# Kernel tuning notes

Hardware: AMD Instinct MI355X
Metric: run time of the kernel (lower is better)

## Reference

```python
import jax, jax.numpy as jnp
import numpy as np

N = 100000   # nodes
E = 1600000  # edges
DIN = 32     # node_in_channels
DE = 16      # edge_feature_dim
H = 64       # gnn_hidden_channels
L = 4        # num_gnn_layers
MH = 128     # mlp_hidden_channels
OUT = 10     # out_channels_final
G = 128      # graphs in batch
BN_EPS = 1e-5
GIN_EPS = 0.0


def setup_inputs() -> dict:
    key = jax.random.key(0)
    ks = jax.random.split(key, 24)
    s = 0.05
    return dict(
        x=jax.random.normal(ks[0], (N, DIN), jnp.float32),
        edge_index=jax.random.randint(ks[1], (2, E), 0, N),
        edge_attr=jax.random.normal(ks[2], (E, DE), jnp.float32),
        batch=jnp.sort(jax.random.randint(ks[3], (N,), 0, G)),
        # layer 0 (in = DIN)
        l0_edge_w=jax.random.normal(ks[4], (DIN, DE), jnp.float32) * s,
        l0_edge_b=jnp.zeros((DIN,), jnp.float32),
        l0_w1=jax.random.normal(ks[5], (H, DIN), jnp.float32) * s,
        l0_b1=jnp.zeros((H,), jnp.float32),
        l0_w2=jax.random.normal(ks[6], (H, H), jnp.float32) * s,
        l0_b2=jnp.zeros((H,), jnp.float32),
        # layers 1..L-1 stacked (in = H)
        edge_w=jax.random.normal(ks[7], (L - 1, H, DE), jnp.float32) * s,
        edge_b=jnp.zeros((L - 1, H), jnp.float32),
        w1=jax.random.normal(ks[8], (L - 1, H, H), jnp.float32) * s,
        b1=jnp.zeros((L - 1, H), jnp.float32),
        w2=jax.random.normal(ks[9], (L - 1, H, H), jnp.float32) * s,
        b2=jnp.zeros((L - 1, H), jnp.float32),
        # batchnorm params, all layers
        bn_gamma=jnp.ones((L, H), jnp.float32),
        bn_beta=jnp.zeros((L, H), jnp.float32),
        # classifier head
        head_w1=jax.random.normal(ks[10], (MH, H), jnp.float32) * s,
        head_b1=jnp.zeros((MH,), jnp.float32),
        head_w2=jax.random.normal(ks[11], (OUT, MH), jnp.float32) * s,
        head_b2=jnp.zeros((OUT,), jnp.float32),
    )


def _gine_layer(x, src, dst, edge_attr, ew, eb, w1, b1, w2, b2, g, beta):
    # message: relu(x_j + Lin(edge_attr)); aggregate: scatter-add at dst
    m = jax.nn.relu(x[src] + edge_attr @ ew.T + eb)           # [E, C]
    agg = jax.ops.segment_sum(m, dst, num_segments=x.shape[0])  # [N, C]
    h = (1.0 + GIN_EPS) * x + agg
    # GINE nn: Linear -> ReLU -> Linear -> ReLU
    h = jax.nn.relu(h @ w1.T + b1)
    h = jax.nn.relu(h @ w2.T + b2)
    # BatchNorm1d (training-mode batch stats, biased variance)
    mu = h.mean(axis=0)
    var = ((h - mu) ** 2).mean(axis=0)
    h = (h - mu) * jax.lax.rsqrt(var + BN_EPS) * g + beta
    return jax.nn.relu(h)


def reference(x, edge_index, edge_attr, batch,
              l0_edge_w, l0_edge_b, l0_w1, l0_b1, l0_w2, l0_b2,
              edge_w, edge_b, w1, b1, w2, b2,
              bn_gamma, bn_beta,
              head_w1, head_b1, head_w2, head_b2):
    src, dst = edge_index[0], edge_index[1]
    h = _gine_layer(x, src, dst, edge_attr, l0_edge_w, l0_edge_b,
                    l0_w1, l0_b1, l0_w2, l0_b2, bn_gamma[0], bn_beta[0])
    for i in range(L - 1):
        h = _gine_layer(h, src, dst, edge_attr, edge_w[i], edge_b[i],
                        w1[i], b1[i], w2[i], b2[i],
                        bn_gamma[i + 1], bn_beta[i + 1])
    # global mean pool over graphs
    sums = jax.ops.segment_sum(h, batch, num_segments=G)           # [G, H]
    cnt = jax.ops.segment_sum(jnp.ones((h.shape[0],), h.dtype), batch, num_segments=G)
    pooled = sums / jnp.maximum(cnt, 1.0)[:, None]
    # MLP head (dropout = identity in eval)
    z = jax.nn.relu(pooled @ head_w1.T + head_b1)
    logits = z @ head_w2.T + head_b2
    return logits
```

## Files before the change

kernel.cpp:

```cpp
#include <hip/hip_runtime.h>
#include <hip/hip_fp16.h>

#define NN 100000
#define NE 1600000
#define DIN 32
#define DE 16
#define HC 64
#define NL 4
#define MHC 128
#define OUTC 10
#define NG 128

typedef _Float16 half4_t __attribute__((ext_vector_type(4)));
typedef float f32x4 __attribute__((ext_vector_type(4)));

__global__ __launch_bounds__(256) void k_deg(const int* __restrict__ dst, int* __restrict__ deg) {
  int e = blockIdx.x * 256 + threadIdx.x;
  if (e < NE) atomicAdd(&deg[dst[e]], 1);
}

__global__ __launch_bounds__(1024) void k_scan1(const int* __restrict__ deg, int* __restrict__ offs, int* __restrict__ bsum) {
  __shared__ int s[1024];
  int t = threadIdx.x;
  int i = blockIdx.x * 1024 + t;
  int v = (i < NN) ? deg[i] : 0;
  s[t] = v; __syncthreads();
  for (int d = 1; d < 1024; d <<= 1) {
    int x = 0;
    if (t >= d) x = s[t - d];
    __syncthreads();
    if (t >= d) s[t] += x;
    __syncthreads();
  }
  if (i < NN) offs[i] = s[t] - v;
  if (t == 1023) bsum[blockIdx.x] = s[t];
}

__global__ __launch_bounds__(128) void k_scan2(int* __restrict__ bsum, int nb) {
  __shared__ int s[128];
  int t = threadIdx.x;
  int v = (t < nb) ? bsum[t] : 0;
  s[t] = v; __syncthreads();
  for (int d = 1; d < 128; d <<= 1) {
    int x = 0;
    if (t >= d) x = s[t - d];
    __syncthreads();
    if (t >= d) s[t] += x;
    __syncthreads();
  }
  if (t < nb) bsum[t] = s[t] - v;
}

__global__ __launch_bounds__(256) void k_scan3(int* __restrict__ offs, const int* __restrict__ bsum,
                                               const int* __restrict__ deg,
                                               int* __restrict__ cur, int2* __restrict__ odeg) {
  int i = blockIdx.x * 256 + threadIdx.x;
  if (i < NN) {
    int o = offs[i] + bsum[i >> 10];
    offs[i] = o;
    cur[i] = o;
    odeg[i] = make_int2(o, deg[i]);
  }
}

__global__ __launch_bounds__(256) void k_fillcast(const int* __restrict__ src, const int* __restrict__ dst,
                                                  int* __restrict__ cur,
                                                  const float4* __restrict__ eattr4,
                                                  int* __restrict__ csrc, uint4* __restrict__ e16) {
  int e = blockIdx.x * 256 + threadIdx.x;
  if (e >= NE) return;
  int d = dst[e];
  float4 a0 = eattr4[(size_t)e * 4 + 0];
  float4 a1 = eattr4[(size_t)e * 4 + 1];
  float4 a2 = eattr4[(size_t)e * 4 + 2];
  float4 a3 = eattr4[(size_t)e * 4 + 3];
  int s = src[e];
  int pos = atomicAdd(&cur[d], 1);
  __half2 h0 = __floats2half2_rn(a0.x, a0.y), h1 = __floats2half2_rn(a0.z, a0.w);
  __half2 h2 = __floats2half2_rn(a1.x, a1.y), h3 = __floats2half2_rn(a1.z, a1.w);
  __half2 h4 = __floats2half2_rn(a2.x, a2.y), h5 = __floats2half2_rn(a2.z, a2.w);
  __half2 h6 = __floats2half2_rn(a3.x, a3.y), h7 = __floats2half2_rn(a3.z, a3.w);
  uint4 o0 = make_uint4(*(unsigned*)&h0, *(unsigned*)&h1, *(unsigned*)&h2, *(unsigned*)&h3);
  uint4 o1 = make_uint4(*(unsigned*)&h4, *(unsigned*)&h5, *(unsigned*)&h6, *(unsigned*)&h7);
  csrc[pos] = s;
  e16[(size_t)pos * 2 + 0] = o0;
  e16[(size_t)pos * 2 + 1] = o1;
}

__global__ __launch_bounds__(256) void k_wprep(const float* __restrict__ l0ew, const float* __restrict__ l0eb,
                                               const float* __restrict__ ew, const float* __restrict__ eb,
                                               unsigned* __restrict__ ewmf, float* __restrict__ ebp) {
  int i = blockIdx.x * 256 + threadIdx.x;
  if (i < 2048) {
    int j = i & 1;
    int l = (i >> 1) & 63;
    int g = (i >> 7) & 3;
    int L = i >> 9;
    int ch = 16 * g + (l & 15);
    int k0 = 4 * (l >> 4) + 2 * j;
    float a, b;
    if (L == 0) {
      a = (ch < 32) ? l0ew[ch * 16 + k0] : 0.f;
      b = (ch < 32) ? l0ew[ch * 16 + k0 + 1] : 0.f;
    } else {
      a = ew[(size_t)(L - 1) * 1024 + ch * 16 + k0];
      b = ew[(size_t)(L - 1) * 1024 + ch * 16 + k0 + 1];
    }
    __half2 h = __floats2half2_rn(a, b);
    ewmf[i] = *(unsigned*)&h;
  }
  if (i < 256) {
    int L = i >> 6, c = i & 63;
    ebp[i] = (L == 0) ? ((c < 32) ? l0eb[c] : 0.f) : eb[(size_t)(L - 1) * 64 + c];
  }
}

__global__ __launch_bounds__(256) void k_wmlp(const float* __restrict__ l0w1, const float* __restrict__ w1,
                                              const float* __restrict__ l0w2, const float* __restrict__ w2,
                                              unsigned* __restrict__ wB) {
  int id = blockIdx.x * 256 + threadIdx.x;
  if (id >= 16384) return;
  int j = id & 1;
  int l = (id >> 1) & 63;
  int cg = (id >> 7) & 3;
  int kb = (id >> 9) & 3;
  int mat = (id >> 11) & 1;
  int L = (id >> 12) & 3;
  int k0 = kb * 16 + 4 * (l >> 4) + 2 * j;
  int c = cg * 16 + (l & 15);
  float a, b;
  if (mat == 0) {
    if (L == 0) {
      a = (k0 < 32) ? l0w1[c * 32 + k0] : 0.f;
      b = (k0 + 1 < 32) ? l0w1[c * 32 + k0 + 1] : 0.f;
    } else {
      a = w1[(size_t)(L - 1) * 4096 + c * 64 + k0];
      b = w1[(size_t)(L - 1) * 4096 + c * 64 + k0 + 1];
    }
  } else {
    if (L == 0) {
      a = l0w2[c * 64 + k0];
      b = l0w2[c * 64 + k0 + 1];
    } else {
      a = w2[(size_t)(L - 1) * 4096 + c * 64 + k0];
      b = w2[(size_t)(L - 1) * 4096 + c * 64 + k0 + 1];
    }
  }
  __half2 h = __floats2half2_rn(a, b);
  wB[id] = *(unsigned*)&h;
}

__global__ __launch_bounds__(256) void k_gstart(const int* __restrict__ batch, int* __restrict__ gstart) {
  int i = blockIdx.x * 256 + threadIdx.x;
  if (i >= NN) return;
  int b = batch[i];
  int bp = (i == 0) ? -1 : batch[i - 1];
  for (int g = bp + 1; g <= b; g++) gstart[g] = i;
  if (i == NN - 1)
    for (int g = b + 1; g <= NG; g++) gstart[g] = NN;
}

__global__ __launch_bounds__(256) void k_xpad16(const float* __restrict__ x, _Float16* __restrict__ xg16) {
  int i = blockIdx.x * 256 + threadIdx.x;
  if (i >= NN * 64) return;
  int row = i >> 6, c = i & 63;
  float v = (c < 32) ? x[(size_t)row * 32 + c] : 0.f;
  xg16[(size_t)row * 64 + (c & 15) * 4 + (c >> 4)] = (_Float16)v;
}

__global__ __launch_bounds__(256) void k_bnapply(const float* __restrict__ h2,
                                                 const float* __restrict__ sc, const float* __restrict__ sh,
                                                 _Float16* __restrict__ xg16) {
  int i = blockIdx.x * 256 + threadIdx.x;
  if (i >= NN * 64) return;
  int row = i >> 6, c = i & 63;
  float v = fmaxf(fmaf(h2[i], sc[c], sh[c]), 0.f);
  xg16[(size_t)row * 64 + (c & 15) * 4 + (c >> 4)] = (_Float16)v;
}

__global__ __launch_bounds__(256) void k_edgeH(
    const int* __restrict__ csrc, const int2* __restrict__ odeg,
    const _Float16* __restrict__ xg16,
    const unsigned* __restrict__ e16,
    const unsigned* __restrict__ ewmf, const float* __restrict__ ebf,
    float* __restrict__ hpre)
{
  int gt = blockIdx.x * 256 + threadIdx.x;
  int node = gt >> 6;
  if (node >= NN) return;
  int c = threadIdx.x & 63;
  int m = c & 15;
  int qv = c >> 4;

  half4_t bf[4];
  #pragma unroll
  for (int g = 0; g < 4; g++) {
    uint2 wv = *(const uint2*)(ewmf + (size_t)(g * 64 + c) * 2);
    bf[g] = __builtin_bit_cast(half4_t, wv);
  }
  float bb[4];
  #pragma unroll
  for (int g = 0; g < 4; g++) bb[g] = ebf[16 * g + m];
  int2 od = odeg[node];
  int start = od.x, n = od.y;
  float acc[4] = {0.f, 0.f, 0.f, 0.f};

  for (int base = 0; base < n; base += 16) {
    int cn = n - base;
    int p = start + base;
    uint2 av = *(const uint2*)(e16 + (size_t)(p + m) * 8 + qv * 2);
    half4_t af = __builtin_bit_cast(half4_t, av);
    f32x4 d0, d1, d2, d3;
    {
      f32x4 ci;
      ci[0] = bb[0]; ci[1] = bb[0]; ci[2] = bb[0]; ci[3] = bb[0];
      d0 = __builtin_amdgcn_mfma_f32_16x16x16f16(af, bf[0], ci, 0, 0, 0);
      ci[0] = bb[1]; ci[1] = bb[1]; ci[2] = bb[1]; ci[3] = bb[1];
      d1 = __builtin_amdgcn_mfma_f32_16x16x16f16(af, bf[1], ci, 0, 0, 0);
      ci[0] = bb[2]; ci[1] = bb[2]; ci[2] = bb[2]; ci[3] = bb[2];
      d2 = __builtin_amdgcn_mfma_f32_16x16x16f16(af, bf[2], ci, 0, 0, 0);
      ci[0] = bb[3]; ci[1] = bb[3]; ci[2] = bb[3]; ci[3] = bb[3];
      d3 = __builtin_amdgcn_mfma_f32_16x16x16f16(af, bf[3], ci, 0, 0, 0);
    }
    int sidx = csrc[p + m];
    #pragma unroll
    for (int r = 0; r < 4; r++) {
      int s = __shfl(sidx, 4 * qv + r);
      bool valid = (4 * qv + r) < cn;
      uint2 xv = *(const uint2*)(xg16 + (size_t)s * 64 + m * 4);
      half4_t hx = __builtin_bit_cast(half4_t, xv);
      #pragma unroll
      for (int g = 0; g < 4; g++) {
        float xs = (float)hx[g];
        float el = (r == 0) ? ((g == 0) ? d0[0] : (g == 1) ? d1[0] : (g == 2) ? d2[0] : d3[0])
                 : (r == 1) ? ((g == 0) ? d0[1] : (g == 1) ? d1[1] : (g == 2) ? d2[1] : d3[1])
                 : (r == 2) ? ((g == 0) ? d0[2] : (g == 1) ? d1[2] : (g == 2) ? d2[2] : d3[2])
                 :            ((g == 0) ? d0[3] : (g == 1) ? d1[3] : (g == 2) ? d2[3] : d3[3]);
        float v = fmaxf(xs + el, 0.f);
        acc[g] += valid ? v : 0.f;
      }
    }
  }
  #pragma unroll
  for (int g = 0; g < 4; g++) {
    acc[g] += __shfl_xor(acc[g], 16);
    acc[g] += __shfl_xor(acc[g], 32);
  }
  float xself = (float)xg16[(size_t)node * 64 + (c & 15) * 4 + (c >> 4)];
  float sum = (qv == 0) ? acc[0] : (qv == 1) ? acc[1] : (qv == 2) ? acc[2] : acc[3];
  hpre[(size_t)node * 64 + c] = xself + sum;
}

__global__ __launch_bounds__(256) void k_mlp(
    const float* __restrict__ hpre,
    const unsigned* __restrict__ wBL,
    const float* __restrict__ b1f, const float* __restrict__ b2v,
    float* __restrict__ h2, float* __restrict__ bnsq)
{
  __shared__ _Float16 ml[64 * 72];
  int tid = threadIdx.x;
  int cg = __builtin_amdgcn_readfirstlane(tid >> 6);
  int l = tid & 63;
  int m = l & 15;
  int q = l >> 4;
  int rbase = blockIdx.x * 64;
  int col = cg * 16 + m;

  uint2 w1f[4], w2f[4];
  #pragma unroll
  for (int kb = 0; kb < 4; kb++) {
    w1f[kb] = *(const uint2*)(wBL + (size_t)(((0 * 4 + kb) * 4 + cg) * 64 + l) * 2);
    w2f[kb] = *(const uint2*)(wBL + (size_t)(((1 * 4 + kb) * 4 + cg) * 64 + l) * 2);
  }
  float b1c = b1f[col], b2c = b2v[col];

  #pragma unroll
  for (int rg = 0; rg < 4; rg++) {
    int row = rbase + rg * 16 + m;
    const float* hp = hpre + (size_t)(row < NN ? row : (NN - 1)) * 64 + 4 * q;
    f32x4 hv0 = *(const f32x4*)(hp + 0);
    f32x4 hv1 = *(const f32x4*)(hp + 16);
    f32x4 hv2 = *(const f32x4*)(hp + 32);
    f32x4 hv3 = *(const f32x4*)(hp + 48);
    f32x4 acc; acc[0] = b1c; acc[1] = b1c; acc[2] = b1c; acc[3] = b1c;
    half4_t a0, a1, a2, a3;
    #pragma unroll
    for (int i = 0; i < 4; i++) {
      a0[i] = (_Float16)hv0[i]; a1[i] = (_Float16)hv1[i];
      a2[i] = (_Float16)hv2[i]; a3[i] = (_Float16)hv3[i];
    }
    acc = __builtin_amdgcn_mfma_f32_16x16x16f16(a0, __builtin_bit_cast(half4_t, w1f[0]), acc, 0, 0, 0);
    acc = __builtin_amdgcn_mfma_f32_16x16x16f16(a1, __builtin_bit_cast(half4_t, w1f[1]), acc, 0, 0, 0);
    acc = __builtin_amdgcn_mfma_f32_16x16x16f16(a2, __builtin_bit_cast(half4_t, w1f[2]), acc, 0, 0, 0);
    acc = __builtin_amdgcn_mfma_f32_16x16x16f16(a3, __builtin_bit_cast(half4_t, w1f[3]), acc, 0, 0, 0);
    #pragma unroll
    for (int i = 0; i < 4; i++)
      ml[(rg * 16 + q * 4 + i) * 72 + col] = (_Float16)fmaxf(acc[i], 0.f);
  }
  __syncthreads();
  float sacc = 0.f, qacc = 0.f;
  #pragma unroll
  for (int rg = 0; rg < 4; rg++) {
    f32x4 acc; acc[0] = b2c; acc[1] = b2c; acc[2] = b2c; acc[3] = b2c;
    #pragma unroll
    for (int kb = 0; kb < 4; kb++) {
      half4_t a = *(const half4_t*)(ml + (rg * 16 + m) * 72 + kb * 16 + 4 * q);
      acc = __builtin_amdgcn_mfma_f32_16x16x16f16(a, __builtin_bit_cast(half4_t, w2f[kb]), acc, 0, 0, 0);
    }
    #pragma unroll
    for (int i = 0; i < 4; i++) {
      int row = rbase + rg * 16 + q * 4 + i;
      bool rok = row < NN;
      float v = rok ? fmaxf(acc[i], 0.f) : 0.f;
      if (rok) h2[(size_t)row * 64 + col] = v;
      sacc += v; qacc += v * v;
    }
  }
  sacc += __shfl_xor(sacc, 16); sacc += __shfl_xor(sacc, 32);
  qacc += __shfl_xor(qacc, 16); qacc += __shfl_xor(qacc, 32);
  int cp = (blockIdx.x & 31) * 128;
  if (q == 0) {
    atomicAdd(&bnsq[cp + col], sacc);
    atomicAdd(&bnsq[cp + 64 + col], qacc);
  }
}

__global__ __launch_bounds__(64) void k_bnfin(const float* __restrict__ bnsq,
                                              const float* __restrict__ gamma, const float* __restrict__ beta,
                                              int layer, float* __restrict__ scs, float* __restrict__ shs) {
  int c = threadIdx.x;
  if (c >= 64) return;
  const float* sl = bnsq + (size_t)layer * 4096;
  float s = 0.f, q = 0.f;
  for (int cp = 0; cp < 32; cp++) { s += sl[cp * 128 + c]; q += sl[cp * 128 + 64 + c]; }
  float mu = s * (1.0f / NN);
  float var = q * (1.0f / NN) - mu * mu;
  float r = rsqrtf(var + 1e-5f);
  float g = gamma[layer * 64 + c] * r;
  scs[layer * 64 + c] = g;
  shs[layer * 64 + c] = beta[layer * 64 + c] - mu * g;
}

__global__ __launch_bounds__(256) void k_pool2(const float* __restrict__ h2, const float* __restrict__ sc,
                                               const float* __restrict__ sh, const int* __restrict__ gstart,
                                               float* __restrict__ pooled) {
  int g = blockIdx.x >> 2, sub = blockIdx.x & 3;
  int s = gstart[g], e = gstart[g + 1];
  int c = threadIdx.x & 63, rg = threadIdx.x >> 6;
  float scv = sc[c], shv = sh[c];
  float acc = 0.f;
  for (int r = s + sub * 4 + rg; r < e; r += 16)
    acc += fmaxf(fmaf(h2[(size_t)r * 64 + c], scv, shv), 0.f);
  __shared__ float ls[256];
  ls[threadIdx.x] = acc;
  __syncthreads();
  if (rg == 0) {
    float v = ls[c] + ls[64 + c] + ls[128 + c] + ls[192 + c];
    atomicAdd(&pooled[g * 64 + c], v);
  }
}

__global__ __launch_bounds__(128) void k_head(const float* __restrict__ pooled, const int* __restrict__ gstart,
                                              const float* __restrict__ hw1, const float* __restrict__ hb1,
                                              const float* __restrict__ hw2, const float* __restrict__ hb2,
                                              float* __restrict__ out) {
  __shared__ float p[64];
  __shared__ float z[128];
  int g = blockIdx.x, t = threadIdx.x;
  if (t < 64) {
    int cn = gstart[g + 1] - gstart[g];
    float inv = 1.0f / (float)(cn > 0 ? cn : 1);
    p[t] = pooled[g * 64 + t] * inv;
  }
  __syncthreads();
  float a = hb1[t];
  #pragma unroll
  for (int k = 0; k < 64; k++) a = fmaf(hw1[t * 64 + k], p[k], a);
  z[t] = fmaxf(a, 0.f);
  __syncthreads();
  if (t < OUTC) {
    float b = hb2[t];
    #pragma unroll
    for (int k = 0; k < 128; k++) b = fmaf(hw2[t * 128 + k], z[k], b);
    out[g * OUTC + t] = b;
  }
}

extern "C" void kernel_launch(void* const* d_in, const int* in_sizes, int n_in,
                              void* d_out, int out_size, void* d_ws, size_t ws_size,
                              hipStream_t stream) {
  const float* x_f   = (const float*)d_in[0];
  const int*   ei    = (const int*)d_in[1];
  const float* eattr = (const float*)d_in[2];
  const int*   batch = (const int*)d_in[3];
  const float* l0_ew = (const float*)d_in[4];
  const float* l0_eb = (const float*)d_in[5];
  const float* l0_w1 = (const float*)d_in[6];
  const float* l0_b1 = (const float*)d_in[7];
  const float* l0_w2 = (const float*)d_in[8];
  const float* l0_b2 = (const float*)d_in[9];
  const float* ew    = (const float*)d_in[10];
  const float* eb    = (const float*)d_in[11];
  const float* w1    = (const float*)d_in[12];
  const float* b1    = (const float*)d_in[13];
  const float* w2    = (const float*)d_in[14];
  const float* b2    = (const float*)d_in[15];
  const float* bng   = (const float*)d_in[16];
  const float* bnb   = (const float*)d_in[17];
  const float* hw1   = (const float*)d_in[18];
  const float* hb1   = (const float*)d_in[19];
  const float* hw2   = (const float*)d_in[20];
  const float* hb2   = (const float*)d_in[21];
  const int* esrc = ei;
  const int* edst = ei + NE;

  char* wsb = (char*)d_ws;
  size_t off = 0;
  auto A = [&](size_t bytes) -> void* {
    void* p = wsb + off;
    off = (off + bytes + 255) & ~(size_t)255;
    return p;
  };
  int*   csrc = (int*)A((size_t)(NE + 16) * 4);
  int*   offs = (int*)A((size_t)NN * 4);
  int*   deg  = (int*)A((size_t)NN * 4);
  int*   cur  = (int*)A((size_t)NN * 4);
  int2*  odeg = (int2*)A((size_t)NN * 8);
  int*   bsum = (int*)A(128 * 4);
  int*   gst  = (int*)A((NG + 1) * 4);
  _Float16* xg16 = (_Float16*)A((size_t)NN * 64 * 2);
  float* hpre = (float*)A((size_t)NN * 64 * 4);
  float* h2   = (float*)A((size_t)NN * 64 * 4);
  float* bnsq = (float*)A(4 * 32 * 128 * 4);
  float* scs  = (float*)A(4 * 64 * 4);
  float* shs  = (float*)A(4 * 64 * 4);
  float* pooled = (float*)A((size_t)NG * 64 * 4);
  unsigned* wB   = (unsigned*)A(16384 * 4);
  unsigned* ewmf = (unsigned*)A(2048 * 4);
  float* ebp  = (float*)A(256 * 4);
  unsigned* e16 = (unsigned*)A(((size_t)NE + 16) * 32);

  hipMemsetAsync(deg, 0, (size_t)NN * 4, stream);
  hipMemsetAsync(bnsq, 0, 4 * 32 * 128 * 4, stream);
  hipMemsetAsync(pooled, 0, (size_t)NG * 64 * 4, stream);
  hipMemsetAsync(csrc + NE, 0, 16 * 4, stream);
  hipMemsetAsync((char*)e16 + (size_t)NE * 32, 0, 16 * 32, stream);

  k_wmlp<<<64, 256, 0, stream>>>(l0_w1, w1, l0_w2, w2, wB);
  k_wprep<<<8, 256, 0, stream>>>(l0_ew, l0_eb, ew, eb, ewmf, ebp);
  k_xpad16<<<(NN * 64 + 255) / 256, 256, 0, stream>>>(x_f, xg16);
  k_gstart<<<(NN + 255) / 256, 256, 0, stream>>>(batch, gst);

  k_deg<<<(NE + 255) / 256, 256, 0, stream>>>(edst, deg);
  k_scan1<<<98, 1024, 0, stream>>>(deg, offs, bsum);
  k_scan2<<<1, 128, 0, stream>>>(bsum, 98);
  k_scan3<<<(NN + 255) / 256, 256, 0, stream>>>(offs, bsum, deg, cur, odeg);
  k_fillcast<<<(NE + 255) / 256, 256, 0, stream>>>(esrc, edst, cur, (const float4*)eattr,
                                                   csrc, (uint4*)e16);

  const int nodeBlocks = (NN * 64 + 255) / 256;
  const int rowBlocks = (NN + 63) / 64;
  const int elemBlocks = (NN * 64 + 255) / 256;

  k_edgeH<<<nodeBlocks, 256, 0, stream>>>(csrc, odeg, xg16, e16, ewmf, ebp, hpre);
  k_mlp<<<rowBlocks, 256, 0, stream>>>(hpre, wB, l0_b1, l0_b2, h2, bnsq + 0);
  k_bnfin<<<1, 64, 0, stream>>>(bnsq, bng, bnb, 0, scs, shs);

  for (int i = 0; i < 3; i++) {
    k_bnapply<<<elemBlocks, 256, 0, stream>>>(h2, scs + i * 64, shs + i * 64, xg16);
    k_edgeH<<<nodeBlocks, 256, 0, stream>>>(csrc, odeg, xg16,
                                            e16, ewmf + (size_t)(i + 1) * 512, ebp + (i + 1) * 64, hpre);
    k_mlp<<<rowBlocks, 256, 0, stream>>>(hpre, wB + (size_t)(i + 1) * 4096, b1 + (size_t)i * 64,
                                         b2 + (size_t)i * 64, h2, bnsq + (size_t)(i + 1) * 4096);
    k_bnfin<<<1, 64, 0, stream>>>(bnsq, bng, bnb, i + 1, scs, shs);
  }

  k_pool2<<<NG * 4, 256, 0, stream>>>(h2, scs + 3 * 64, shs + 3 * 64, gst, pooled);
  k_head<<<NG, 128, 0, stream>>>(pooled, gst, hw1, hb1, hw2, hb2, (float*)d_out);
}
```

Before: 834.9 us.

## Fuse edge aggregation and node MLP into one per-layer kernel

Merges the edge message/aggregation kernel with the MLP kernel so aggregated node features stay in shared memory instead of going through a global hpre buffer. Each wave now processes 16 nodes sequentially, filling a 64-row tile, then the block runs the two MFMA linear layers on it. This removes a global write/read round trip and one launch per layer, but cuts the number of waves and serializes node gathers within a wave, which may reduce latency hiding.

```diff
diff --git a/kernel.cpp b/kernel.cpp
--- a/kernel.cpp
+++ b/kernel.cpp
@@ -178,85 +178,16 @@
   xg16[(size_t)row * 64 + (c & 15) * 4 + (c >> 4)] = (_Float16)v;
 }
 
-__global__ __launch_bounds__(256) void k_edgeH(
+__global__ __launch_bounds__(256) void k_layer(
     const int* __restrict__ csrc, const int2* __restrict__ odeg,
     const _Float16* __restrict__ xg16,
     const unsigned* __restrict__ e16,
     const unsigned* __restrict__ ewmf, const float* __restrict__ ebf,
-    float* __restrict__ hpre)
-{
-  int gt = blockIdx.x * 256 + threadIdx.x;
-  int node = gt >> 6;
-  if (node >= NN) return;
-  int c = threadIdx.x & 63;
-  int m = c & 15;
-  int qv = c >> 4;
-
-  half4_t bf[4];
-  #pragma unroll
-  for (int g = 0; g < 4; g++) {
-    uint2 wv = *(const uint2*)(ewmf + (size_t)(g * 64 + c) * 2);
-    bf[g] = __builtin_bit_cast(half4_t, wv);
-  }
-  float bb[4];
-  #pragma unroll
-  for (int g = 0; g < 4; g++) bb[g] = ebf[16 * g + m];
-  int2 od = odeg[node];
-  int start = od.x, n = od.y;
-  float acc[4] = {0.f, 0.f, 0.f, 0.f};
-
-  for (int base = 0; base < n; base += 16) {
-    int cn = n - base;
-    int p = start + base;
-    uint2 av = *(const uint2*)(e16 + (size_t)(p + m) * 8 + qv * 2);
-    half4_t af = __builtin_bit_cast(half4_t, av);
-    f32x4 d0, d1, d2, d3;
-    {
-      f32x4 ci;
-      ci[0] = bb[0]; ci[1] = bb[0]; ci[2] = bb[0]; ci[3] = bb[0];
-      d0 = __builtin_amdgcn_mfma_f32_16x16x16f16(af, bf[0], ci, 0, 0, 0);
-      ci[0] = bb[1]; ci[1] = bb[1]; ci[2] = bb[1]; ci[3] = bb[1];
-      d1 = __builtin_amdgcn_mfma_f32_16x16x16f16(af, bf[1], ci, 0, 0, 0);
-      ci[0] = bb[2]; ci[1] = bb[2]; ci[2] = bb[2]; ci[3] = bb[2];
-      d2 = __builtin_amdgcn_mfma_f32_16x16x16f16(af, bf[2], ci, 0, 0, 0);
-      ci[0] = bb[3]; ci[1] = bb[3]; ci[2] = bb[3]; ci[3] = bb[3];
-      d3 = __builtin_amdgcn_mfma_f32_16x16x16f16(af, bf[3], ci, 0, 0, 0);
-    }
-    int sidx = csrc[p + m];
-    #pragma unroll
-    for (int r = 0; r < 4; r++) {
-      int s = __shfl(sidx, 4 * qv + r);
-      bool valid = (4 * qv + r) < cn;
-      uint2 xv = *(const uint2*)(xg16 + (size_t)s * 64 + m * 4);
-      half4_t hx = __builtin_bit_cast(half4_t, xv);
-      #pragma unroll
-      for (int g = 0; g < 4; g++) {
-        float xs = (float)hx[g];
-        float el = (r == 0) ? ((g == 0) ? d0[0] : (g == 1) ? d1[0] : (g == 2) ? d2[0] : d3[0])
-                 : (r == 1) ? ((g == 0) ? d0[1] : (g == 1) ? d1[1] : (g == 2) ? d2[1] : d3[1])
-                 : (r == 2) ? ((g == 0) ? d0[2] : (g == 1) ? d1[2] : (g == 2) ? d2[2] : d3[2])
-                 :            ((g == 0) ? d0[3] : (g == 1) ? d1[3] : (g == 2) ? d2[3] : d3[3]);
-        float v = fmaxf(xs + el, 0.f);
-        acc[g] += valid ? v : 0.f;
-      }
-    }
-  }
-  #pragma unroll
-  for (int g = 0; g < 4; g++) {
-    acc[g] += __shfl_xor(acc[g], 16);
-    acc[g] += __shfl_xor(acc[g], 32);
-  }
-  float xself = (float)xg16[(size_t)node * 64 + (c & 15) * 4 + (c >> 4)];
-  float sum = (qv == 0) ? acc[0] : (qv == 1) ? acc[1] : (qv == 2) ? acc[2] : acc[3];
-  hpre[(size_t)node * 64 + c] = xself + sum;
-}
-
-__global__ __launch_bounds__(256) void k_mlp(
-    const float* __restrict__ hpre,
     const unsigned* __restrict__ wBL,
     const float* __restrict__ b1f, const float* __restrict__ b2v,
     float* __restrict__ h2, float* __restrict__ bnsq)
 {
+  __shared__ float hl[64 * 68];
   __shared__ _Float16 ml[64 * 72];
   int tid = threadIdx.x;
   int cg = __builtin_amdgcn_readfirstlane(tid >> 6);
@@ -266,6 +197,15 @@
   int rbase = blockIdx.x * 64;
   int col = cg * 16 + m;
 
+  half4_t bf[4];
+  #pragma unroll
+  for (int g = 0; g < 4; g++) {
+    uint2 wv = *(const uint2*)(ewmf + (size_t)(g * 64 + l) * 2);
+    bf[g] = __builtin_bit_cast(half4_t, wv);
+  }
+  float bb[4];
+  #pragma unroll
+  for (int g = 0; g < 4; g++) bb[g] = ebf[16 * g + m];
   uint2 w1f[4], w2f[4];
   #pragma unroll
   for (int kb = 0; kb < 4; kb++) {
@@ -274,10 +214,65 @@
   }
   float b1c = b1f[col], b2c = b2v[col];
 
+  for (int t = 0; t < 16; t++) {
+    int node = rbase + cg * 16 + t;
+    float hv = 0.f;
+    if (node < NN) {
+      int2 od = odeg[node];
+      int start = od.x, n = od.y;
+      float acc[4] = {0.f, 0.f, 0.f, 0.f};
+      for (int base = 0; base < n; base += 16) {
+        int cn = n - base;
+        int p = start + base;
+        uint2 av = *(const uint2*)(e16 + (size_t)(p + m) * 8 + q * 2);
+        half4_t af = __builtin_bit_cast(half4_t, av);
+        f32x4 d0, d1, d2, d3;
+        {
+          f32x4 ci;
+          ci[0] = bb[0]; ci[1] = bb[0]; ci[2] = bb[0]; ci[3] = bb[0];
+          d0 = __builtin_amdgcn_mfma_f32_16x16x16f16(af, bf[0], ci, 0, 0, 0);
+          ci[0] = bb[1]; ci[1] = bb[1]; ci[2] = bb[1]; ci[3] = bb[1];
+          d1 = __builtin_amdgcn_mfma_f32_16x16x16f16(af, bf[1], ci, 0, 0, 0);
+          ci[0] = bb[2]; ci[1] = bb[2]; ci[2] = bb[2]; ci[3] = bb[2];
+          d2 = __builtin_amdgcn_mfma_f32_16x16x16f16(af, bf[2], ci, 0, 0, 0);
+          ci[0] = bb[3]; ci[1] = bb[3]; ci[2] = bb[3]; ci[3] = bb[3];
+          d3 = __builtin_amdgcn_mfma_f32_16x16x16f16(af, bf[3], ci, 0, 0, 0);
+        }
+        int sidx = csrc[p + m];
+        #pragma unroll
+        for (int r = 0; r < 4; r++) {
+          int s = __shfl(sidx, 4 * q + r);
+          bool valid = (4 * q + r) < cn;
+          uint2 xv = *(const uint2*)(xg16 + (size_t)s * 64 + m * 4);
+          half4_t hx = __builtin_bit_cast(half4_t, xv);
+          #pragma unroll
+          for (int g = 0; g < 4; g++) {
+            float xs = (float)hx[g];
+            float el = (r == 0) ? ((g == 0) ? d0[0] : (g == 1) ? d1[0] : (g == 2) ? d2[0] : d3[0])
+                     : (r == 1) ? ((g == 0) ? d0[1] : (g == 1) ? d1[1] : (g == 2) ? d2[1] : d3[1])
+                     : (r == 2) ? ((g == 0) ? d0[2] : (g == 1) ? d1[2] : (g == 2) ? d2[2] : d3[2])
+                     :            ((g == 0) ? d0[3] : (g == 1) ? d1[3] : (g == 2) ? d2[3] : d3[3]);
+            float v = fmaxf(xs + el, 0.f);
+            acc[g] += valid ? v : 0.f;
+          }
+        }
+      }
+      #pragma unroll
+      for (int g = 0; g < 4; g++) {
+        acc[g] += __shfl_xor(acc[g], 16);
+        acc[g] += __shfl_xor(acc[g], 32);
+      }
+      float xself = (float)xg16[(size_t)node * 64 + (l & 15) * 4 + (l >> 4)];
+      float sum = (q == 0) ? acc[0] : (q == 1) ? acc[1] : (q == 2) ? acc[2] : acc[3];
+      hv = xself + sum;
+    }
+    hl[(cg * 16 + t) * 68 + l] = hv;
+  }
+  __syncthreads();
+
   #pragma unroll
   for (int rg = 0; rg < 4; rg++) {
-    int row = rbase + rg * 16 + m;
-    const float* hp = hpre + (size_t)(row < NN ? row : (NN - 1)) * 64 + 4 * q;
+    const float* hp = hl + (rg * 16 + m) * 68 + 4 * q;
     f32x4 hv0 = *(const f32x4*)(hp + 0);
     f32x4 hv1 = *(const f32x4*)(hp + 16);
     f32x4 hv2 = *(const f32x4*)(hp + 32);
@@ -298,6 +293,7 @@
       ml[(rg * 16 + q * 4 + i) * 72 + col] = (_Float16)fmaxf(acc[i], 0.f);
   }
   __syncthreads();
+
   float sacc = 0.f, qacc = 0.f;
   #pragma unroll
   for (int rg = 0; rg < 4; rg++) {
@@ -429,7 +425,6 @@
   int*   bsum = (int*)A(128 * 4);
   int*   gst  = (int*)A((NG + 1) * 4);
   _Float16* xg16 = (_Float16*)A((size_t)NN * 64 * 2);
-  float* hpre = (float*)A((size_t)NN * 64 * 4);
   float* h2   = (float*)A((size_t)NN * 64 * 4);
   float* bnsq = (float*)A(4 * 32 * 128 * 4);
   float* scs  = (float*)A(4 * 64 * 4);
@@ -458,20 +453,19 @@
   k_fillcast<<<(NE + 255) / 256, 256, 0, stream>>>(esrc, edst, cur, (const float4*)eattr,
                                                    csrc, (uint4*)e16);
 
-  const int nodeBlocks = (NN * 64 + 255) / 256;
   const int rowBlocks = (NN + 63) / 64;
   const int elemBlocks = (NN * 64 + 255) / 256;
 
-  k_edgeH<<<nodeBlocks, 256, 0, stream>>>(csrc, odeg, xg16, e16, ewmf, ebp, hpre);
-  k_mlp<<<rowBlocks, 256, 0, stream>>>(hpre, wB, l0_b1, l0_b2, h2, bnsq + 0);
+  k_layer<<<rowBlocks, 256, 0, stream>>>(csrc, odeg, xg16, e16, ewmf, ebp,
+                                         wB, l0_b1, l0_b2, h2, bnsq + 0);
   k_bnfin<<<1, 64, 0, stream>>>(bnsq, bng, bnb, 0, scs, shs);
 
   for (int i = 0; i < 3; i++) {
     k_bnapply<<<elemBlocks, 256, 0, stream>>>(h2, scs + i * 64, shs + i * 64, xg16);
-    k_edgeH<<<nodeBlocks, 256, 0, stream>>>(csrc, odeg, xg16,
-                                            e16, ewmf + (size_t)(i + 1) * 512, ebp + (i + 1) * 64, hpre);
-    k_mlp<<<rowBlocks, 256, 0, stream>>>(hpre, wB + (size_t)(i + 1) * 4096, b1 + (size_t)i * 64,
-                                         b2 + (size_t)i * 64, h2, bnsq + (size_t)(i + 1) * 4096);
+    k_layer<<<rowBlocks, 256, 0, stream>>>(csrc, odeg, xg16,
+                                           e16, ewmf + (size_t)(i + 1) * 512, ebp + (i + 1) * 64,
+                                           wB + (size_t)(i + 1) * 4096, b1 + (size_t)i * 64,
+                                           b2 + (size_t)i * 64, h2, bnsq + (size_t)(i + 1) * 4096);
     k_bnfin<<<1, 64, 0, stream>>>(bnsq, bng, bnb, i + 1, scs, shs);
   }
 
```

Result: faster. 731.1 us (-12.4%).
